# Performance work log

Hardware: AMD Instinct MI355X
Metric: run time of the kernel (lower is better)

## Reference

```python
import jax, jax.numpy as jnp
import numpy as np

K = 8          # kernels per group
H = 32         # groups (g // divisor)
NUM_DIL = 14   # int(log2((75000-1)/8)) + 1


def _gconv1d(x, w, d, p):
    # x: (B, H, T), w: (H*K, 1, 9) grouped conv, dilation d, padding p
    return jax.lax.conv_general_dilated(
        x, w, window_strides=(1,), padding=[(p, p)], rhs_dilation=(d,),
        dimension_numbers=("NCH", "OIH", "NCH"), feature_group_count=H)


def setup_inputs() -> dict:
    key = jax.random.key(0)
    kX, kW, kI = jax.random.split(key, 3)
    X = jax.random.normal(kX, (4, 17, 75000), dtype=jnp.float32)
    W = jax.random.normal(kW, (NUM_DIL, 2, K * H, 1, 9), dtype=jnp.float32)
    W = W - W.mean(-1, keepdims=True)
    W = W / jnp.abs(W).sum(-1, keepdims=True)
    idx = jax.random.randint(kI, (NUM_DIL, 2, H, 8), 0, 17, dtype=jnp.int32)
    return {"X": X, "W": W, "idx": idx}


def reference(X, W, idx):
    B = X.shape[0]
    diff_X = jnp.diff(X, axis=-1)  # (B, C, T-1)
    bi = jnp.arange(B)[:, None, None]
    hi = jnp.arange(H)[None, :, None]
    outs = []
    for di in range(NUM_DIL):
        d = 2 ** di
        p = 4 * d  # (9-1)*d // 2
        for diff_i in range(2):
            src = X if diff_i == 0 else diff_X
            # channel gather + sum: (B, H, 8, T) -> (B, H, T)
            g = src[:, idx[di, diff_i]].sum(2)
            z = _gconv1d(g, W[di, diff_i], d, p)  # (B, H*K, L)
            z = z.reshape(B, H, K, -1)            # (B, H, K, L)
            max_v = z.max(2)                       # (B, H, L)
            max_i = z.argmax(2)
            min_i = z.argmin(2)
            count_max = jnp.zeros((B, H, K), z.dtype).at[bi, hi, max_i].add(max_v)
            count_min = jnp.zeros((B, H, K), z.dtype).at[bi, hi, min_i].add(1.0)
            outs.append(count_max)
            outs.append(count_min)
    return jnp.concatenate(outs, axis=1).reshape(B, -1)  # (B, 14336)
```

## Files before the change

### kernel.cpp

```cpp
#include <hip/hip_runtime.h>

typedef float F2 __attribute__((ext_vector_type(2)));

#define NB 4
#define NC 17
#define T0 75000
#define NH 32
#define NK 8

__global__ void diffK(const float* __restrict__ X, float* __restrict__ D) {
    int t = blockIdx.x * 256 + threadIdx.x;
    int row = blockIdx.y;
    if (t < T0) {
        size_t o = (size_t)row * T0 + t;
        D[o] = (t < T0 - 1) ? (X[o + 1] - X[o]) : 0.f;
    }
}

__device__ __forceinline__ float packK(float z, int k) {
    unsigned u = (__float_as_uint(z) & 0xFFFFFFF8u) | (unsigned)k;
    return __uint_as_float(u);
}

__device__ __forceinline__ void pkfma_lo(F2& z, F2 g, unsigned long long w) {
    asm("v_pk_fma_f32 %0, %1, %2, %0 op_sel:[0,0,0] op_sel_hi:[1,0,1]"
        : "+v"(z) : "v"(g), "s"(w));
}
__device__ __forceinline__ void pkfma_hi(F2& z, F2 g, unsigned long long w) {
    asm("v_pk_fma_f32 %0, %1, %2, %0 op_sel:[0,1,0] op_sel_hi:[1,1,1]"
        : "+v"(z) : "v"(g), "s"(w));
}
__device__ __forceinline__ void pkmul_lo(F2& z, F2 g, unsigned long long w) {
    asm("v_pk_mul_f32 %0, %1, %2 op_sel:[0,0] op_sel_hi:[1,0]"
        : "=v"(z) : "v"(g), "s"(w));
}
__device__ __forceinline__ void pkmul_hi(F2& z, F2 g, unsigned long long w) {
    asm("v_pk_mul_f32 %0, %1, %2 op_sel:[0,1] op_sel_hi:[1,1]"
        : "=v"(z) : "v"(g), "s"(w));
}

template <int C>
__device__ __forceinline__ void epi8(const F2* Z, float* accM, unsigned long long& cnt) {
    float p[8];
#pragma unroll
    for (int k = 0; k < 8; ++k) p[k] = packK(C ? Z[k].y : Z[k].x, k);
    float ma = fmaxf(fmaxf(p[0], p[1]), p[2]);
    float mb = fmaxf(fmaxf(p[3], p[4]), p[5]);
    float mc = fmaxf(fmaxf(p[6], p[7]), ma);
    float best = fmaxf(mb, mc);
    float na = fminf(fminf(p[0], p[1]), p[2]);
    float nb = fminf(fminf(p[3], p[4]), p[5]);
    float nc = fminf(fminf(p[6], p[7]), na);
    float worst = fminf(nb, nc);
    int biK = __float_as_uint(best) & 7;
    int wiK = __float_as_uint(worst) & 7;
#pragma unroll
    for (int k = 0; k < 8; ++k) accM[k] += (k == biK) ? best : 0.f;
    cnt += 1ull << (wiK << 3);
}

__device__ __forceinline__ void conv9(F2* Z, const F2* g9, const unsigned long long* wq) {
#pragma unroll
    for (int k = 0; k < 8; ++k) {
        const int wi = k * 9;
        if (wi & 1) pkmul_hi(Z[k], g9[0], wq[wi >> 1]);
        else        pkmul_lo(Z[k], g9[0], wq[wi >> 1]);
    }
#pragma unroll
    for (int j = 1; j < 9; ++j) {
#pragma unroll
        for (int k = 0; k < 8; ++k) {
            const int wi = k * 9 + j;
            if (wi & 1) pkfma_hi(Z[k], g9[j], wq[wi >> 1]);
            else        pkfma_lo(Z[k], g9[j], wq[wi >> 1]);
        }
    }
}

constexpr int TS = 2048;
constexpr int A_TILES = 37;
constexpr int A_BLOCKS_PER_G = 128 * A_TILES;
constexpr int A_GROUPS = 12;
constexpr int A_TOTAL_BLOCKS = A_GROUPS * A_BLOCKS_PER_G;

template <bool USE_D>
__global__ __launch_bounds__(256) void kernA(const float* __restrict__ X,
                                             const float* __restrict__ Dws,
                                             const float* __restrict__ Wt,
                                             const int* __restrict__ idx,
                                             float* __restrict__ out) {
    __shared__ float Sbuf[16 * 257];
    __shared__ float red[4][16];

    const int tid = threadIdx.x;
    const int bid = blockIdx.x;
    const int ga = bid / A_BLOCKS_PER_G;
    const int rem = bid - ga * A_BLOCKS_PER_G;
    const int b = rem & 3;
    const int z = rem >> 2;
    const int h = z & 31;
    const int tile = z >> 5;
    const int di = ga >> 1, diff = ga & 1;
    const int d = 1 << di;
    const int T = T0 - diff;
    const int t0 = tile * TS;
    const int span = TS + 8 * d;
    const int g0 = t0 - 4 * d;

    const int* ip = idx + (ga * NH + h) * 8;
    int offs[8];
#pragma unroll
    for (int i = 0; i < 8; ++i)
        offs[i] = __builtin_amdgcn_readfirstlane((b * NC + ip[i]) * T0);

    if (USE_D) {
        const float* base = diff ? Dws : X;
        for (int e = tid * 2; e < span; e += 512) {
            int u = g0 + e;
            F2 s = {0.f, 0.f};
            if (u >= 0 && u + 1 < T0) {
#pragma unroll
                for (int i = 0; i < 8; ++i) s += *(const F2*)(base + offs[i] + u);
            } else {
#pragma unroll
                for (int c = 0; c < 2; ++c) {
                    int uc = u + c;
                    float sc = 0.f;
                    if (uc >= 0 && uc < T0) {
#pragma unroll
                        for (int i = 0; i < 8; ++i) sc += base[offs[i] + uc];
                    }
                    s[c] = sc;
                }
            }
            if (e + 1 < span) *(F2*)(Sbuf + e) = s;
            else Sbuf[e] = s.x;
        }
    } else {
        for (int ls = tid; ls < span; ls += 256) {
            int u = g0 + ls;
            float s = 0.f;
            if (diff) {
                if (u >= 0 && u < T0 - 1) {
#pragma unroll
                    for (int i = 0; i < 8; ++i) s += X[offs[i] + u + 1] - X[offs[i] + u];
                }
            } else {
                if (u >= 0 && u < T0) {
#pragma unroll
                    for (int i = 0; i < 8; ++i) s += X[offs[i] + u];
                }
            }
            Sbuf[ls] = s;
        }
    }
    __syncthreads();

    const int wbase = __builtin_amdgcn_readfirstlane((ga * (NK * NH) + h * NK) * 9);
    const unsigned long long* wq64 = (const unsigned long long*)(Wt + wbase);
    unsigned long long wq[36];
#pragma unroll
    for (int i = 0; i < 36; ++i) wq[i] = wq64[i];

    float accM[8];
#pragma unroll
    for (int k = 0; k < 8; ++k) accM[k] = 0.f;
    unsigned long long cnt = 0;

#pragma unroll
    for (int it = 0; it < 4; ++it) {
        int p = tid + it * 256;
        int t = t0 + p;
        F2 g9[9];
#pragma unroll
        for (int j = 0; j < 9; ++j) {
            g9[j].x = Sbuf[p + j * d];
            g9[j].y = Sbuf[p + 1024 + j * d];
        }
        F2 Z[8];
        conv9(Z, g9, wq);
        if (t < T)        epi8<0>(Z, accM, cnt);
        if (t + 1024 < T) epi8<1>(Z, accM, cnt);
    }

    float accC[8];
#pragma unroll
    for (int k = 0; k < 8; ++k) accC[k] = (float)((unsigned)(cnt >> (k * 8)) & 255u);

    __syncthreads();
#pragma unroll
    for (int k = 0; k < 8; ++k) {
        Sbuf[k * 257 + tid] = accM[k];
        Sbuf[(k + 8) * 257 + tid] = accC[k];
    }
    __syncthreads();
    {
        int k = tid & 15, seg = tid >> 4;
        const float* rp = Sbuf + k * 257 + seg * 16;
        float s = 0.f;
#pragma unroll
        for (int i = 0; i < 16; ++i) s += rp[i];
        s += __shfl_xor(s, 16, 64);
        s += __shfl_xor(s, 32, 64);
        int wv = tid >> 6;
        if ((tid & 63) < 16) red[wv][k] = s;
    }
    __syncthreads();
    if (tid < 16) {
        float v = red[0][tid] + red[1][tid] + red[2][tid] + red[3][tid];
        int which = tid >> 3;
        int k = tid & 7;
        int o = ga * 2 + which;
        atomicAdd(&out[(size_t)b * 14336 + (o * NH + h) * NK + k], v);
    }
}

struct BG2 { int base, segs2, di, diff; };
constexpr BG2 BGS2[16] = {
    {0,     640,  6, 0}, {320,   640,  6, 1},
    {640,   640,  7, 0}, {960,   640,  7, 1},
    {1280,  640,  8, 0}, {1600,  640,  8, 1},
    {1920,  768,  9, 0}, {2304,  768,  9, 1},
    {2688, 1024, 10, 0}, {3200, 1024, 10, 1},
    {3712, 1024, 11, 0}, {4224, 1024, 11, 1},
    {4736, 2048, 12, 0}, {5760, 2048, 12, 1},
    {6784, 4096, 13, 0}, {8832, 4096, 13, 1},
};
constexpr int B2_BLOCKS = 10880;

template <bool USE_D>
__device__ __forceinline__ F2 gather2(const float* __restrict__ base,
                                      const int* offs, int u, int diffF) {
    F2 s = {0.f, 0.f};
    if (u >= 0 && u + 1 < T0) {
        if (!USE_D && diffF) {
            float m0 = 0.f, m1 = 0.f, m2 = 0.f;
#pragma unroll
            for (int i = 0; i < 8; ++i) {
                m0 += base[offs[i] + u];
                m1 += base[offs[i] + u + 1];
                m2 += (u + 2 < T0) ? base[offs[i] + u + 2] : base[offs[i] + u + 1];
            }
            s.x = m1 - m0;
            s.y = (u + 2 < T0) ? (m2 - m1) : 0.f;
        } else {
#pragma unroll
            for (int i = 0; i < 8; ++i) s += *(const F2*)(base + offs[i] + u);
        }
    } else if (u + 1 >= 0 && u < T0) {
#pragma unroll
        for (int c = 0; c < 2; ++c) {
            int uc = u + c;
            float sc = 0.f;
            if (uc >= 0 && uc < T0) {
                if (!USE_D && diffF) {
                    if (uc < T0 - 1) {
#pragma unroll
                        for (int i = 0; i < 8; ++i)
                            sc += base[offs[i] + uc + 1] - base[offs[i] + uc];
                    }
                } else {
#pragma unroll
                    for (int i = 0; i < 8; ++i) sc += base[offs[i] + uc];
                }
            }
            s[c] = sc;
        }
    }
    return s;
}

template <bool USE_D>
__global__ __launch_bounds__(256, 4) void kernB2(const float* __restrict__ X,
                                                 const float* __restrict__ Dws,
                                                 const float* __restrict__ Wt,
                                                 const int* __restrict__ idx,
                                                 float* __restrict__ out) {
    const int tid = threadIdx.x;
    const int bid = blockIdx.x;

    int di = 6, diff = 0, gig = 0, combo = 0, sg = 0;
#pragma unroll
    for (int g = 0; g < 16; ++g) {
        const int s2 = BGS2[g].segs2;
        if (bid >= BGS2[g].base && bid < BGS2[g].base + 128 * s2 / 256) {
            gig = (bid - BGS2[g].base) * 256 + tid;
            combo = gig / s2;
            sg = gig - combo * s2;
            di = BGS2[g].di; diff = BGS2[g].diff;
        }
    }
    combo = __builtin_amdgcn_readfirstlane(combo);
    di    = __builtin_amdgcn_readfirstlane(di);
    diff  = __builtin_amdgcn_readfirstlane(diff);

    const int d = 1 << di;
    const int T = T0 - diff;
    const int Q = (T + d - 1) >> di;
    const int ga = di * 2 + diff;
    const int b = combo & 3;
    const int h = combo >> 2;

    const int p = sg & ((d >> 1) - 1);
    const int q0 = (sg >> (di - 1)) * 60;
    const int r = 2 * p;

    const int* ip = idx + (ga * NH + h) * 8;
    int offs[8];
#pragma unroll
    for (int i = 0; i < 8; ++i)
        offs[i] = __builtin_amdgcn_readfirstlane((b * NC + ip[i]) * T0);

    const int wbase = __builtin_amdgcn_readfirstlane((ga * (NK * NH) + h * NK) * 9);
    const unsigned long long* wq64 = (const unsigned long long*)(Wt + wbase);
    unsigned long long wq[36];
#pragma unroll
    for (int i = 0; i < 36; ++i) wq[i] = wq64[i];

    const float* base = (USE_D && diff) ? Dws : X;

    float accM[8];
#pragma unroll
    for (int k = 0; k < 8; ++k) accM[k] = 0.f;
    unsigned long long cnt = 0;

    const int t0 = r + q0 * d;
    F2 buf[12];
    {
        int u = t0 - 4 * d;
#pragma unroll
        for (int m = 0; m < 12; ++m) { buf[m] = gather2<USE_D>(base, offs, u, diff); u += d; }
    }

    for (int outer = 0; outer < 5; ++outer) {
        if (q0 + outer * 12 >= Q) break;
        const int tb = t0 + outer * 12 * d;
#pragma unroll
        for (int ii = 0; ii < 12; ++ii) {
            const int t = tb + ii * d;
            F2 g9[9];
#pragma unroll
            for (int j = 0; j < 9; ++j) g9[j] = buf[(ii + j) % 12];
            F2 Z[8];
            conv9(Z, g9, wq);
            if (t < T)     epi8<0>(Z, accM, cnt);
            if (t + 1 < T) epi8<1>(Z, accM, cnt);
            buf[ii] = gather2<USE_D>(base, offs, t + 8 * d, diff);
        }
    }

    float accC[8];
#pragma unroll
    for (int k = 0; k < 8; ++k) accC[k] = (float)((unsigned)(cnt >> (k * 8)) & 255u);

#pragma unroll
    for (int k = 0; k < 8; ++k) {
#pragma unroll
        for (int sh = 1; sh < 64; sh <<= 1) {
            accM[k] += __shfl_xor(accM[k], sh, 64);
            accC[k] += __shfl_xor(accC[k], sh, 64);
        }
    }
    if ((tid & 63) == 0) {
        size_t bb = (size_t)b * 14336;
        int o = ga * 2;
#pragma unroll
        for (int k = 0; k < 8; ++k) {
            atomicAdd(&out[bb + (o * NH + h) * NK + k],       accM[k]);
            atomicAdd(&out[bb + ((o + 1) * NH + h) * NK + k], accC[k]);
        }
    }
}

__global__ void zeroK(float* __restrict__ out, int n) {
    int i = blockIdx.x * 256 + threadIdx.x;
    if (i < n) out[i] = 0.f;
}

extern "C" void kernel_launch(void* const* d_in, const int* in_sizes, int n_in,
                              void* d_out, int out_size, void* d_ws, size_t ws_size,
                              hipStream_t stream) {
    const float* X  = (const float*)d_in[0];
    const float* Wt = (const float*)d_in[1];
    const int*  idx = (const int*)d_in[2];
    float* out = (float*)d_out;
    float* Dws = (float*)d_ws;

    const size_t D_BYTES = (size_t)NB * NC * T0 * sizeof(float);
    const bool useD = ws_size >= D_BYTES;

    zeroK<<<(out_size + 255) / 256, 256, 0, stream>>>(out, out_size);
    if (useD) {
        dim3 dg((T0 + 255) / 256, NB * NC);
        diffK<<<dg, 256, 0, stream>>>(X, Dws);
        kernA<true><<<A_TOTAL_BLOCKS, 256, 0, stream>>>(X, Dws, Wt, idx, out);
        kernB2<true><<<B2_BLOCKS, 256, 0, stream>>>(X, Dws, Wt, idx, out);
    } else {
        kernA<false><<<A_TOTAL_BLOCKS, 256, 0, stream>>>(X, Dws, Wt, idx, out);
        kernB2<false><<<B2_BLOCKS, 256, 0, stream>>>(X, Dws, Wt, idx, out);
    }
}
```

Measured before the change: 939.9 us.

## Accumulate argmax/argmin bins with per-wave shared-memory atomics instead of registers

```diff
diff --git a/kernel.cpp b/kernel.cpp
--- a/kernel.cpp
+++ b/kernel.cpp
@@ -40,7 +40,8 @@
 }
 
 template <int C>
-__device__ __forceinline__ void epi8(const F2* Z, float* accM, unsigned long long& cnt) {
+__device__ __forceinline__ void epiB(const F2* Z, float* __restrict__ bM,
+                                     unsigned* __restrict__ bC) {
     float p[8];
 #pragma unroll
     for (int k = 0; k < 8; ++k) p[k] = packK(C ? Z[k].y : Z[k].x, k);
@@ -54,9 +55,8 @@
     float worst = fminf(nb, nc);
     int biK = __float_as_uint(best) & 7;
     int wiK = __float_as_uint(worst) & 7;
-#pragma unroll
-    for (int k = 0; k < 8; ++k) accM[k] += (k == biK) ? best : 0.f;
-    cnt += 1ull << (wiK << 3);
+    atomicAdd(&bM[biK], best);
+    atomicAdd(&bC[wiK], 1u);
 }
 
 __device__ __forceinline__ void conv9(F2* Z, const F2* g9, const unsigned long long* wq) {
@@ -89,8 +89,9 @@
                                              const float* __restrict__ Wt,
                                              const int* __restrict__ idx,
                                              float* __restrict__ out) {
-    __shared__ float Sbuf[16 * 257];
-    __shared__ float red[4][16];
+    __shared__ float Sbuf[TS + 8 * 32 + 2];
+    __shared__ float binsM[4][8];
+    __shared__ unsigned binsC[4][8];
 
     const int tid = threadIdx.x;
     const int bid = blockIdx.x;
@@ -107,6 +108,9 @@
     const int span = TS + 8 * d;
     const int g0 = t0 - 4 * d;
 
+    const int wv = tid >> 6, lane = tid & 63;
+    if (lane < 8) { binsM[wv][lane] = 0.f; binsC[wv][lane] = 0u; }
+
     const int* ip = idx + (ga * NH + h) * 8;
     int offs[8];
 #pragma unroll
@@ -162,11 +166,6 @@
 #pragma unroll
     for (int i = 0; i < 36; ++i) wq[i] = wq64[i];
 
-    float accM[8];
-#pragma unroll
-    for (int k = 0; k < 8; ++k) accM[k] = 0.f;
-    unsigned long long cnt = 0;
-
 #pragma unroll
     for (int it = 0; it < 4; ++it) {
         int p = tid + it * 256;
@@ -179,37 +178,19 @@
         }
         F2 Z[8];
         conv9(Z, g9, wq);
-        if (t < T)        epi8<0>(Z, accM, cnt);
-        if (t + 1024 < T) epi8<1>(Z, accM, cnt);
-    }
-
-    float accC[8];
-#pragma unroll
-    for (int k = 0; k < 8; ++k) accC[k] = (float)((unsigned)(cnt >> (k * 8)) & 255u);
-
-    __syncthreads();
-#pragma unroll
-    for (int k = 0; k < 8; ++k) {
-        Sbuf[k * 257 + tid] = accM[k];
-        Sbuf[(k + 8) * 257 + tid] = accC[k];
-    }
-    __syncthreads();
-    {
-        int k = tid & 15, seg = tid >> 4;
-        const float* rp = Sbuf + k * 257 + seg * 16;
-        float s = 0.f;
-#pragma unroll
-        for (int i = 0; i < 16; ++i) s += rp[i];
-        s += __shfl_xor(s, 16, 64);
-        s += __shfl_xor(s, 32, 64);
-        int wv = tid >> 6;
-        if ((tid & 63) < 16) red[wv][k] = s;
-    }
+        if (t < T)        epiB<0>(Z, binsM[wv], binsC[wv]);
+        if (t + 1024 < T) epiB<1>(Z, binsM[wv], binsC[wv]);
+    }
+
     __syncthreads();
     if (tid < 16) {
-        float v = red[0][tid] + red[1][tid] + red[2][tid] + red[3][tid];
         int which = tid >> 3;
         int k = tid & 7;
+        float v;
+        if (which == 0)
+            v = binsM[0][k] + binsM[1][k] + binsM[2][k] + binsM[3][k];
+        else
+            v = (float)(binsC[0][k] + binsC[1][k] + binsC[2][k] + binsC[3][k]);
         int o = ga * 2 + which;
         atomicAdd(&out[(size_t)b * 14336 + (o * NH + h) * NK + k], v);
     }
@@ -276,8 +257,14 @@
                                                  const float* __restrict__ Wt,
                                                  const int* __restrict__ idx,
                                                  float* __restrict__ out) {
+    __shared__ float binsM[4][8];
+    __shared__ unsigned binsC[4][8];
+
     const int tid = threadIdx.x;
     const int bid = blockIdx.x;
+    const int wv = tid >> 6, lane = tid & 63;
+
+    if (lane < 8) { binsM[wv][lane] = 0.f; binsC[wv][lane] = 0u; }
 
     int di = 6, diff = 0, gig = 0, combo = 0, sg = 0;
 #pragma unroll
@@ -319,11 +306,6 @@
 
     const float* base = (USE_D && diff) ? Dws : X;
 
-    float accM[8];
-#pragma unroll
-    for (int k = 0; k < 8; ++k) accM[k] = 0.f;
-    unsigned long long cnt = 0;
-
     const int t0 = r + q0 * d;
     F2 buf[12];
     {
@@ -343,32 +325,20 @@
             for (int j = 0; j < 9; ++j) g9[j] = buf[(ii + j) % 12];
             F2 Z[8];
             conv9(Z, g9, wq);
-            if (t < T)     epi8<0>(Z, accM, cnt);
-            if (t + 1 < T) epi8<1>(Z, accM, cnt);
+            if (t < T)     epiB<0>(Z, binsM[wv], binsC[wv]);
+            if (t + 1 < T) epiB<1>(Z, binsM[wv], binsC[wv]);
             buf[ii] = gather2<USE_D>(base, offs, t + 8 * d, diff);
         }
     }
 
-    float accC[8];
-#pragma unroll
-    for (int k = 0; k < 8; ++k) accC[k] = (float)((unsigned)(cnt >> (k * 8)) & 255u);
-
-#pragma unroll
-    for (int k = 0; k < 8; ++k) {
-#pragma unroll
-        for (int sh = 1; sh < 64; sh <<= 1) {
-            accM[k] += __shfl_xor(accM[k], sh, 64);
-            accC[k] += __shfl_xor(accC[k], sh, 64);
-        }
-    }
-    if ((tid & 63) == 0) {
+    {
         size_t bb = (size_t)b * 14336;
         int o = ga * 2;
-#pragma unroll
-        for (int k = 0; k < 8; ++k) {
-            atomicAdd(&out[bb + (o * NH + h) * NK + k],       accM[k]);
-            atomicAdd(&out[bb + ((o + 1) * NH + h) * NK + k], accC[k]);
-        }
+        if (lane < 8)
+            atomicAdd(&out[bb + (o * NH + h) * NK + lane], binsM[wv][lane]);
+        else if (lane < 16)
+            atomicAdd(&out[bb + ((o + 1) * NH + h) * NK + (lane & 7)],
+                      (float)binsC[wv][lane & 7]);
     }
 }
 
```

Result: slower. 1.864 ms (+98.3%).
